# Kernel tuning notes

Measured on AMD Instinct MI355X. Metric: run time of the kernel, lower is better.

## Reference

```python
import jax, jax.numpy as jnp
import numpy as np
from jax import lax

N = 5000          # num atoms
E = 4             # num edge types
DIM_H = 128
VOCAB = 100       # num_atoms_vocab; embedding table has VOCAB+1 rows
T = 4             # max_time_steps


def setup_inputs() -> dict:
    key = jax.random.key(0)
    k1, k2, k3, k4 = jax.random.split(key, 4)
    atom_arr = jax.random.randint(k1, (N,), 0, VOCAB, dtype=jnp.int64 if jax.config.read('jax_enable_x64') else jnp.int32)
    adjs = jax.random.randint(k2, (E, N, N), 0, 2, dtype=jnp.int32)
    # learned parameters
    embedding = jax.random.normal(k3, (VOCAB + 1, DIM_H), dtype=jnp.float32) * 0.05
    limit = float(np.sqrt(6.0 / (DIM_H + DIM_H)))  # glorot uniform
    H_edges = jax.random.uniform(k4, (E, DIM_H, DIM_H), minval=-limit, maxval=limit, dtype=jnp.float32)
    return {
        "atom_arr": atom_arr,
        "adjs": adjs,
        "max_time_steps": T,
        "embedding": embedding,
        "H_edges": H_edges,
    }


def reference(atom_arr, adjs, max_time_steps, embedding, H_edges):
    # h_v^0 = embedding lookup, [N, H]
    h0 = embedding[atom_arr]
    # adjacency mask as float, [E, N, N]
    A = (adjs == 1).astype(h0.dtype)

    def step(h, _):
        # original: for each node v, edge type e: H_e @ sum_{u: adj[e,v,u]==1} h_u
        agg = jnp.einsum('evu,uh->evh', A, h)          # neighbor sum per edge type
        msg = jnp.einsum('eij,evj->vi', H_edges, agg)  # edge-type transform + sum over e
        h_new = jax.nn.sigmoid(h + msg)
        return h_new, h_new

    _, h_all = lax.scan(step, h0, None, length=max_time_steps)
    return h_all  # [T, N, H]
```

## Files before the change

### kernel.cpp

```cpp
#include <hip/hip_runtime.h>

#define NROW 5000
#define NPAD 5120
#define KW   80
#define KC   80
#define KZ   4
#define KCQ  20
#define HDIM 128
#define FXS  4194304.0f
#define PART ((size_t)4 * NROW * HDIM)

typedef _Float16 f16x8 __attribute__((ext_vector_type(8)));
typedef float f32x16 __attribute__((ext_vector_type(16)));

__device__ __forceinline__ unsigned short f2h_int(int v) {
    union { _Float16 h; unsigned short u; } c;
    c.h = (_Float16)(float)v;
    return c.u;
}
__device__ __forceinline__ void fx_digits(float h, unsigned short& d1, unsigned short& d0) {
    int q = (int)rintf(h * FXS);
    d1 = f2h_int(q >> 11);
    d0 = f2h_int(q & 2047);
}

__device__ __forceinline__ size_t bt_idx(int kc, int pl, int kk, int half, int col, int j) {
    return (((((size_t)kc * 2 + pl) * 4 + kk) * 2 + half) * 128 + col) * 8 + j;
}

__global__ __launch_bounds__(256) void prep_atom_kernel(const unsigned int* __restrict__ atomw,
                                                        int* __restrict__ atomIdx) {
    __shared__ int s_is64;
    if (threadIdx.x == 0) {
        bool all0 = true, anynz = false;
        for (int j = 0; j < 64; ++j) {
            unsigned lo = atomw[2 * j], hi = atomw[2 * j + 1];
            all0 = all0 && (hi == 0u);
            anynz = anynz || (lo != 0u);
        }
        s_is64 = (all0 && anynz) ? 1 : 0;
    }
    __syncthreads();
    int v = blockIdx.x * 256 + threadIdx.x;
    if (v < NROW) atomIdx[v] = s_is64 ? (int)atomw[2 * v] : (int)atomw[v];
}

__global__ __launch_bounds__(256) void prep_pack_kernel(const int* __restrict__ adjs,
                                                        unsigned long long* __restrict__ packedR) {
    const int er = blockIdx.x;
    const int e = er / NPAD;
    const int r = er - e * NPAD;
    const int wave = threadIdx.x >> 6;
    const int lane = threadIdx.x & 63;
    const int* rowp = adjs + ((size_t)e * NROW + r) * NROW;
    unsigned long long* outp = packedR + ((size_t)e * NPAD + r) * KW;
    const bool rok = (r < NROW);
    for (int c = wave; c < KW; c += 4) {
        int u = c * 64 + lane;
        int val = (rok && u < NROW) ? rowp[u] : 0;
        unsigned long long m = __ballot(val == 1);
        if (lane == 0) outp[c] = m;
    }
}

__global__ __launch_bounds__(256) void prep_packT_kernel(const unsigned long long* __restrict__ packedR,
                                                         unsigned long long* __restrict__ packedT) {
    __shared__ unsigned long long slds[64][KW + 1];
    const int e = blockIdx.y;
    const int r0 = blockIdx.x * 64;
    const int tid = threadIdx.x;
#pragma unroll
    for (int p = 0; p < 20; ++p) {
        int idx = p * 256 + tid;
        int r = idx / KW;
        int c = idx - r * KW;
        slds[r][c] = packedR[((size_t)e * NPAD + r0 + r) * KW + c];
    }
    __syncthreads();
#pragma unroll
    for (int p = 0; p < 20; ++p) {
        int idx = p * 256 + tid;
        int kc = idx >> 6;
        int rr = idx & 63;
        packedT[((size_t)e * KC + kc) * NPAD + r0 + rr] = slds[rr][kc];
    }
}

__global__ __launch_bounds__(256) void prep_h0T_kernel(const int* __restrict__ atomIdx,
                                                       const float* __restrict__ emb,
                                                       unsigned short* __restrict__ hTt) {
    const int i = blockIdx.y;
    const int v = blockIdx.x * 256 + threadIdx.x;
    float val = 0.f;
    if (v < NROW) val = emb[(size_t)atomIdx[v] * HDIM + i];
    unsigned short d1, d0;
    fx_digits(val, d1, d0);
    const int kc = v >> 6, kk = (v >> 4) & 3, half = (v >> 3) & 1, j = v & 7;
    hTt[bt_idx(kc, 0, kk, half, i, j)] = d1;
    hTt[bt_idx(kc, 1, kk, half, i, j)] = d0;
}

__global__ __launch_bounds__(256) void prep_h0f_kernel(const int* __restrict__ atomIdx,
                                                       const float* __restrict__ emb,
                                                       float* __restrict__ h) {
    int idx = blockIdx.x * 256 + threadIdx.x;
    int v = idx >> 7, i = idx & 127;
    h[idx] = emb[(size_t)atomIdx[v] * HDIM + i];
}

__global__ __launch_bounds__(256) void prep_Ht_kernel(const float* __restrict__ H,
                                                      float* __restrict__ Htr) {
    int idx = blockIdx.x * 256 + threadIdx.x;
    int e = idx >> 14;
    int j = (idx >> 7) & 127;
    int i = idx & 127;
    Htr[idx] = H[((size_t)e * HDIM + i) * HDIM + j];
}

__global__ __launch_bounds__(512, 4) void gemm1_kernel(const unsigned long long* __restrict__ packedT,
                                                       const unsigned short* __restrict__ hTt,
                                                       float* __restrict__ agg) {
    const int m0 = blockIdx.x * 128;
    const int e = blockIdx.y;
    const int kz = blockIdx.z;
    const int tid = threadIdx.x;
    const int lane = tid & 63;
    const int wave = tid >> 6;
    const int wm = wave >> 2;
    const int wc = wave & 3;
    const int l31 = lane & 31;
    const int l1 = lane >> 5;
    const int sh2 = l1 * 8;
    const int col = wc * 32 + l31;
    const int kc0 = kz * KCQ;

    f32x16 acc[2][2];
#pragma unroll
    for (int pl = 0; pl < 2; ++pl)
#pragma unroll
        for (int mt = 0; mt < 2; ++mt) acc[pl][mt] = (f32x16)(0.f);

    const unsigned long long* ap = packedT + ((size_t)e * KC + kc0) * NPAD + m0 + wm * 64 + l31;
    const _Float16* bp = (const _Float16*)hTt + (size_t)kc0 * 16384 +
                         (size_t)l1 * 1024 + (size_t)col * 8;

    for (int kc = 0; kc < KCQ; ++kc) {
        unsigned long long aw[2];
        aw[0] = ap[0];
        aw[1] = ap[32];

        f16x8 bf[2][4];
#pragma unroll
        for (int pl = 0; pl < 2; ++pl)
#pragma unroll
            for (int kk = 0; kk < 4; ++kk)
                bf[pl][kk] = *(const f16x8*)(bp + pl * 8192 + kk * 2048);

        ap += NPAD;
        bp += 16384;

#pragma unroll
        for (int kk = 0; kk < 4; ++kk) {
#pragma unroll
            for (int mt = 0; mt < 2; ++mt) {
                unsigned int w = (kk < 2) ? (unsigned int)aw[mt]
                                          : (unsigned int)(aw[mt] >> 32);
                unsigned int b = (w >> ((kk & 1) * 16 + sh2)) & 0xFFu;
                unsigned int y = b | (b << 15);
                union { unsigned int u[4]; f16x8 h; } Af;
#pragma unroll
                for (int q = 0; q < 4; ++q)
                    Af.u[q] = ((y >> (2 * q)) & 0x00010001u) * 0x3C00u;
#pragma unroll
                for (int pl = 0; pl < 2; ++pl)
                    acc[pl][mt] = __builtin_amdgcn_mfma_f32_32x32x16_f16(
                        Af.h, bf[pl][kk], acc[pl][mt], 0, 0, 0);
            }
        }
    }

    float* aggz = agg + (size_t)kz * PART;
#pragma unroll
    for (int mt = 0; mt < 2; ++mt)
#pragma unroll
        for (int reg = 0; reg < 16; ++reg) {
            int row = (reg & 3) + 8 * (reg >> 2) + 4 * l1;
            int v = m0 + wm * 64 + mt * 32 + row;
            if (v < NROW) {
                double d = (double)acc[0][mt][reg] * 2048.0 + (double)acc[1][mt][reg];
                aggz[((size_t)e * NROW + v) * HDIM + col] = (float)(d * (1.0 / 4194304.0));
            }
        }
}

__global__ __launch_bounds__(256) void gemm2_kernel(const float* __restrict__ agg,
                                                    const float* __restrict__ Htr,
                                                    float* __restrict__ hf,
                                                    float* __restrict__ outp,
                                                    unsigned short* __restrict__ hTt) {
    __shared__ float aggs[8][512];
    __shared__ unsigned short hs[2][128][8];
    const int tid = threadIdx.x;
    const int v0 = blockIdx.x * 8;

#pragma unroll
    for (int it = 0; it < 4; ++it) {
        int idx = it * 256 + tid;
        int r = idx >> 7;
        int c = (idx & 127) * 4;
        int e = c >> 7, j = c & 127;
        size_t o = ((size_t)e * NROW + (v0 + r)) * HDIM + j;
        float4 a0 = *(const float4*)&agg[o];
        float4 a1 = *(const float4*)&agg[PART + o];
        float4 a2 = *(const float4*)&agg[2 * PART + o];
        float4 a3 = *(const float4*)&agg[3 * PART + o];
        *(float4*)&aggs[r][c] = make_float4((a0.x + a1.x) + (a2.x + a3.x),
                                            (a0.y + a1.y) + (a2.y + a3.y),
                                            (a0.z + a1.z) + (a2.z + a3.z),
                                            (a0.w + a1.w) + (a2.w + a3.w));
    }
    __syncthreads();

    const int ip = tid & 63;
    const int vg = tid >> 6;
    const int i0 = ip * 2;

    float m[2][2][4];
#pragma unroll
    for (int r = 0; r < 2; ++r)
#pragma unroll
        for (int q = 0; q < 2; ++q)
#pragma unroll
            for (int k = 0; k < 4; ++k) m[r][q][k] = 0.f;

    const int rb = vg * 2;
    for (int cg = 0; cg < 128; ++cg) {
        int c = cg * 4;
        float4 q0 = *(const float4*)&aggs[rb][c];
        float4 q1 = *(const float4*)&aggs[rb + 1][c];
        float a0v[4] = {q0.x, q0.y, q0.z, q0.w};
        float a1v[4] = {q1.x, q1.y, q1.z, q1.w};
#pragma unroll
        for (int k = 0; k < 4; ++k) {
            float2 w = *(const float2*)&Htr[(size_t)(c + k) * HDIM + i0];
            m[0][0][k] += a0v[k] * w.x;
            m[0][1][k] += a0v[k] * w.y;
            m[1][0][k] += a1v[k] * w.x;
            m[1][1][k] += a1v[k] * w.y;
        }
    }

#pragma unroll
    for (int r = 0; r < 2; ++r) {
        int vr = rb + r;
        int v = v0 + vr;
        size_t o = (size_t)v * HDIM + i0;
        float2 hv = *(const float2*)&hf[o];
        float ms0 = (m[r][0][0] + m[r][0][1]) + (m[r][0][2] + m[r][0][3]);
        float ms1 = (m[r][1][0] + m[r][1][1]) + (m[r][1][2] + m[r][1][3]);
        float x0 = hv.x + ms0;
        float x1 = hv.y + ms1;
        float s0 = 1.0f / (1.0f + expf(-x0));
        float s1 = 1.0f / (1.0f + expf(-x1));
        *(float2*)&outp[o] = make_float2(s0, s1);
        *(float2*)&hf[o] = make_float2(s0, s1);
        unsigned short d1a, d0a, d1b, d0b;
        fx_digits(s0, d1a, d0a);
        fx_digits(s1, d1b, d0b);
        hs[0][i0][vr] = d1a;
        hs[1][i0][vr] = d0a;
        hs[0][i0 + 1][vr] = d1b;
        hs[1][i0 + 1][vr] = d0b;
    }
    __syncthreads();
    if (tid < 128) {
        const int kc = v0 >> 6, kk = (v0 >> 4) & 3, half = (v0 >> 3) & 1;
#pragma unroll
        for (int pl = 0; pl < 2; ++pl)
            *(uint4*)&hTt[bt_idx(kc, pl, kk, half, tid, 0)] = *(const uint4*)&hs[pl][tid][0];
    }
}

extern "C" void kernel_launch(void* const* d_in, const int* in_sizes, int n_in,
                              void* d_out, int out_size, void* d_ws, size_t ws_size,
                              hipStream_t stream) {
    const unsigned int* atomw = (const unsigned int*)d_in[0];
    const int* adjs = (const int*)d_in[1];
    const float* emb = (const float*)d_in[3];
    const float* H = (const float*)d_in[4];
    float* out = (float*)d_out;

    char* ws = (char*)d_ws;
    unsigned long long* packedT = (unsigned long long*)ws;
    size_t off = (size_t)4 * KC * NPAD * 8;
    unsigned short* hTt = (unsigned short*)(ws + off);
    off += (size_t)2 * KC * HDIM * 64 * 2;
    float* hf = (float*)(ws + off);
    off += (size_t)NROW * HDIM * 4;
    float* agg = (float*)(ws + off);
    off += (size_t)KZ * PART * 4;
    float* Htr = (float*)(ws + off);
    off += (size_t)4 * HDIM * HDIM * 4;
    int* atomIdx = (int*)(ws + off);
    off += (size_t)NROW * 4;
    off = (off + 255) & ~(size_t)255;
    unsigned long long* packedR = (unsigned long long*)(ws + off);
    off += (size_t)4 * NPAD * KW * 8;

    prep_atom_kernel<<<dim3((NROW + 255) / 256), 256, 0, stream>>>(atomw, atomIdx);
    prep_pack_kernel<<<dim3(4 * NPAD), 256, 0, stream>>>(adjs, packedR);
    prep_packT_kernel<<<dim3(NPAD / 64, 4), 256, 0, stream>>>(packedR, packedT);
    prep_h0T_kernel<<<dim3(NPAD / 256, HDIM), 256, 0, stream>>>(atomIdx, emb, hTt);
    prep_h0f_kernel<<<dim3(NROW * HDIM / 256), 256, 0, stream>>>(atomIdx, emb, hf);
    prep_Ht_kernel<<<dim3(4 * HDIM * HDIM / 256), 256, 0, stream>>>(H, Htr);

    for (int t = 0; t < 4; ++t) {
        gemm1_kernel<<<dim3(NPAD / 128, 4, KZ), 512, 0, stream>>>(packedT, hTt, agg);
        gemm2_kernel<<<dim3(NROW / 8), 256, 0, stream>>>(agg, Htr, hf,
                                                         out + (size_t)t * NROW * HDIM, hTt);
    }
}
```

Before: 1.051 ms.

## Pre-expand adjacency bits to fp16 operand layout for dense gemm1 path

Adds a prep kernel that expands the bit-packed adjacency once into an fp16 matrix already laid out as MFMA A fragments. A new gemm1 variant loads these fragments directly instead of unpacking bits into fp16 in the inner loop every time step. The dense path is chosen only when the workspace is large enough. It trades per-iteration ALU unpacking for about 16x more A-operand memory traffic (roughly 420 MB read per gemm1 call) plus a large one-time expansion write.

Measured after the change: 1.199 ms. 1.14x slower.

```diff
diff --git a/kernel.cpp b/kernel.cpp
--- a/kernel.cpp
+++ b/kernel.cpp
@@ -26,6 +26,10 @@
 
 __device__ __forceinline__ size_t bt_idx(int kc, int pl, int kk, int half, int col, int j) {
     return (((((size_t)kc * 2 + pl) * 4 + kk) * 2 + half) * 128 + col) * 8 + j;
+}
+
+__device__ __forceinline__ size_t at_idx(int e, int kc, int kk, int half, int row, int j) {
+    return ((((size_t)(e * KC + kc) * 4 + kk) * 2 + half) * NPAD + row) * 8 + j;
 }
 
 __global__ __launch_bounds__(256) void prep_atom_kernel(const unsigned int* __restrict__ atomw,
@@ -86,6 +90,28 @@
     }
 }
 
+__global__ __launch_bounds__(256) void prep_Aexp_kernel(const unsigned long long* __restrict__ packedR,
+                                                        unsigned short* __restrict__ At) {
+    const int row = blockIdx.x * 256 + threadIdx.x;
+    const int kc = blockIdx.y;
+    const int z = blockIdx.z;
+    const int e = z >> 3;
+    const int kk = (z >> 2) & 1 ? 0 : 0;
+    const int kh = z & 7;
+    const int kk2 = kh >> 1;
+    const int half = kh & 1;
+    (void)kk;
+    unsigned long long word = packedR[((size_t)e * NPAD + row) * KW + kc];
+    unsigned int b = (unsigned int)(word >> (kk2 * 16 + half * 8)) & 0xFFu;
+    unsigned int y = b | (b << 15);
+    uint4 u;
+    u.x = ((y >> 0) & 0x00010001u) * 0x3C00u;
+    u.y = ((y >> 2) & 0x00010001u) * 0x3C00u;
+    u.z = ((y >> 4) & 0x00010001u) * 0x3C00u;
+    u.w = ((y >> 6) & 0x00010001u) * 0x3C00u;
+    *(uint4*)&At[at_idx(e, kc, kk2, half, row, 0)] = u;
+}
+
 __global__ __launch_bounds__(256) void prep_h0T_kernel(const int* __restrict__ atomIdx,
                                                        const float* __restrict__ emb,
                                                        unsigned short* __restrict__ hTt) {
@@ -117,9 +143,79 @@
     Htr[idx] = H[((size_t)e * HDIM + i) * HDIM + j];
 }
 
-__global__ __launch_bounds__(512, 4) void gemm1_kernel(const unsigned long long* __restrict__ packedT,
-                                                       const unsigned short* __restrict__ hTt,
-                                                       float* __restrict__ agg) {
+__global__ __launch_bounds__(512, 4) void gemm1_dense_kernel(const unsigned short* __restrict__ At,
+                                                             const unsigned short* __restrict__ hTt,
+                                                             float* __restrict__ agg) {
+    const int m0 = blockIdx.x * 128;
+    const int e = blockIdx.y;
+    const int kz = blockIdx.z;
+    const int tid = threadIdx.x;
+    const int lane = tid & 63;
+    const int wave = tid >> 6;
+    const int wm = wave >> 2;
+    const int wc = wave & 3;
+    const int l31 = lane & 31;
+    const int l1 = lane >> 5;
+    const int col = wc * 32 + l31;
+    const int kc0 = kz * KCQ;
+
+    f32x16 acc[2][2];
+#pragma unroll
+    for (int pl = 0; pl < 2; ++pl)
+#pragma unroll
+        for (int mt = 0; mt < 2; ++mt) acc[pl][mt] = (f32x16)(0.f);
+
+    const _Float16* aD = (const _Float16*)At +
+                         (((size_t)(e * KC + kc0) * 4) * 2 + l1) * ((size_t)NPAD * 8) +
+                         (size_t)(m0 + wm * 64 + l31) * 8;
+    const _Float16* bp = (const _Float16*)hTt + (size_t)kc0 * 16384 +
+                         (size_t)l1 * 1024 + (size_t)col * 8;
+
+    for (int kc = 0; kc < KCQ; ++kc) {
+        f16x8 af[4][2];
+#pragma unroll
+        for (int kk = 0; kk < 4; ++kk)
+#pragma unroll
+            for (int mt = 0; mt < 2; ++mt)
+                af[kk][mt] = *(const f16x8*)(aD + (size_t)kk * 81920 + mt * 256);
+
+        f16x8 bf[2][4];
+#pragma unroll
+        for (int pl = 0; pl < 2; ++pl)
+#pragma unroll
+            for (int kk = 0; kk < 4; ++kk)
+                bf[pl][kk] = *(const f16x8*)(bp + pl * 8192 + kk * 2048);
+
+        aD += 327680;
+        bp += 16384;
+
+#pragma unroll
+        for (int kk = 0; kk < 4; ++kk)
+#pragma unroll
+            for (int mt = 0; mt < 2; ++mt)
+#pragma unroll
+                for (int pl = 0; pl < 2; ++pl)
+                    acc[pl][mt] = __builtin_amdgcn_mfma_f32_32x32x16_f16(
+                        af[kk][mt], bf[pl][kk], acc[pl][mt], 0, 0, 0);
+    }
+
+    float* aggz = agg + (size_t)kz * PART;
+#pragma unroll
+    for (int mt = 0; mt < 2; ++mt)
+#pragma unroll
+        for (int reg = 0; reg < 16; ++reg) {
+            int row = (reg & 3) + 8 * (reg >> 2) + 4 * l1;
+            int v = m0 + wm * 64 + mt * 32 + row;
+            if (v < NROW) {
+                double d = (double)acc[0][mt][reg] * 2048.0 + (double)acc[1][mt][reg];
+                aggz[((size_t)e * NROW + v) * HDIM + col] = (float)(d * (1.0 / 4194304.0));
+            }
+        }
+}
+
+__global__ __launch_bounds__(512, 4) void gemm1_bits_kernel(const unsigned long long* __restrict__ packedT,
+                                                            const unsigned short* __restrict__ hTt,
+                                                            float* __restrict__ agg) {
     const int m0 = blockIdx.x * 128;
     const int e = blockIdx.y;
     const int kz = blockIdx.z;
@@ -148,23 +244,19 @@
         unsigned long long aw[2];
         aw[0] = ap[0];
         aw[1] = ap[32];
-
         f16x8 bf[2][4];
 #pragma unroll
         for (int pl = 0; pl < 2; ++pl)
 #pragma unroll
             for (int kk = 0; kk < 4; ++kk)
                 bf[pl][kk] = *(const f16x8*)(bp + pl * 8192 + kk * 2048);
-
         ap += NPAD;
         bp += 16384;
-
 #pragma unroll
         for (int kk = 0; kk < 4; ++kk) {
 #pragma unroll
             for (int mt = 0; mt < 2; ++mt) {
-                unsigned int w = (kk < 2) ? (unsigned int)aw[mt]
-                                          : (unsigned int)(aw[mt] >> 32);
+                unsigned int w = (kk < 2) ? (unsigned int)aw[mt] : (unsigned int)(aw[mt] >> 32);
                 unsigned int b = (w >> ((kk & 1) * 16 + sh2)) & 0xFFu;
                 unsigned int y = b | (b << 15);
                 union { unsigned int u[4]; f16x8 h; } Af;
@@ -306,16 +398,26 @@
     off = (off + 255) & ~(size_t)255;
     unsigned long long* packedR = (unsigned long long*)(ws + off);
     off += (size_t)4 * NPAD * KW * 8;
+    unsigned short* At = (unsigned short*)(ws + off);
+    size_t off_end = off + (size_t)4 * KC * 8 * NPAD * 8 * 2;
+    const bool dense = (ws_size >= off_end);
 
     prep_atom_kernel<<<dim3((NROW + 255) / 256), 256, 0, stream>>>(atomw, atomIdx);
     prep_pack_kernel<<<dim3(4 * NPAD), 256, 0, stream>>>(adjs, packedR);
-    prep_packT_kernel<<<dim3(NPAD / 64, 4), 256, 0, stream>>>(packedR, packedT);
+    if (dense) {
+        prep_Aexp_kernel<<<dim3(NPAD / 256, KC, 32), 256, 0, stream>>>(packedR, At);
+    } else {
+        prep_packT_kernel<<<dim3(NPAD / 64, 4), 256, 0, stream>>>(packedR, packedT);
+    }
     prep_h0T_kernel<<<dim3(NPAD / 256, HDIM), 256, 0, stream>>>(atomIdx, emb, hTt);
     prep_h0f_kernel<<<dim3(NROW * HDIM / 256), 256, 0, stream>>>(atomIdx, emb, hf);
     prep_Ht_kernel<<<dim3(4 * HDIM * HDIM / 256), 256, 0, stream>>>(H, Htr);
 
     for (int t = 0; t < 4; ++t) {
-        gemm1_kernel<<<dim3(NPAD / 128, 4, KZ), 512, 0, stream>>>(packedT, hTt, agg);
+        if (dense)
+            gemm1_dense_kernel<<<dim3(NPAD / 128, 4, KZ), 512, 0, stream>>>(At, hTt, agg);
+        else
+            gemm1_bits_kernel<<<dim3(NPAD / 128, 4, KZ), 512, 0, stream>>>(packedT, hTt, agg);
         gemm2_kernel<<<dim3(NROW / 8), 256, 0, stream>>>(agg, Htr, hf,
                                                          out + (size_t)t * NROW * HDIM, hTt);
     }
```
